# Performance work log

Hardware: AMD Instinct MI355X
Metric: run time of the kernel (lower is better)

The kernel has to match this reference:

```python
import jax, jax.numpy as jnp
import numpy as np

DIM = 256
HEADS = 8
HEAD_DIM = DIM // HEADS
EPS = 1e-5


def layer_norm(x, g, b):
    mu = jnp.mean(x, axis=-1, keepdims=True)
    var = jnp.mean(jnp.square(x - mu), axis=-1, keepdims=True)
    return (x - mu) * jax.lax.rsqrt(var + EPS) * g + b


def setup_inputs() -> dict:
    key = jax.random.key(0)
    ks = jax.random.split(key, 10)
    s = 0.02
    return {
        "x": jax.random.normal(ks[0], (4, DIM, 64, 64), dtype=jnp.float32),
        "g1": jnp.ones((DIM,), jnp.float32),
        "b1": jnp.zeros((DIM,), jnp.float32),
        "Wqkv": jax.random.normal(ks[1], (DIM, 3 * DIM), jnp.float32) * s,
        "Wp": jax.random.normal(ks[2], (DIM, DIM), jnp.float32) * s,
        "bp": jnp.zeros((DIM,), jnp.float32),
        "g2": jnp.ones((DIM,), jnp.float32),
        "b2": jnp.zeros((DIM,), jnp.float32),
        "W1": jax.random.normal(ks[3], (DIM, 2 * DIM), jnp.float32) * s,
        "bf1": jnp.zeros((2 * DIM,), jnp.float32),
        "W2": jax.random.normal(ks[4], (2 * DIM, DIM), jnp.float32) * s,
        "bf2": jnp.zeros((DIM,), jnp.float32),
    }


def reference(x, g1, b1, Wqkv, Wp, bp, g2, b2, W1, bf1, W2, bf2):
    B, C, H, W = x.shape
    N = H * W
    scale = HEAD_DIM ** -0.5
    tokens = x.reshape(B, C, N).transpose(0, 2, 1)  # [B,N,C]
    t = layer_norm(tokens, g1, b1)
    qkv = (t @ Wqkv).reshape(B, N, 3, HEADS, HEAD_DIM)
    q = qkv[:, :, 0].transpose(0, 2, 1, 3)  # [B,h,N,d]
    k = qkv[:, :, 1].transpose(0, 2, 1, 3)
    v = qkv[:, :, 2].transpose(0, 2, 1, 3)
    attn = jax.nn.softmax(jnp.einsum("bhnd,bhmd->bhnm", q, k) * scale, axis=-1)
    out = jnp.einsum("bhnm,bhmd->bhnd", attn, v)
    out = out.transpose(0, 2, 1, 3).reshape(B, N, C)
    tokens = tokens + out @ Wp + bp
    t2 = layer_norm(tokens, g2, b2)
    h = jax.nn.gelu(t2 @ W1 + bf1, approximate=False)
    tokens = tokens + h @ W2 + bf2
    return tokens.transpose(0, 2, 1).reshape(B, C, H, W)
```

## Files before the change

kernel.cpp:

```cpp
#include <hip/hip_runtime.h>

typedef unsigned short u16;
typedef unsigned int   u32;

using bf16x8 = __attribute__((ext_vector_type(8))) __bf16;
using f32x4  = __attribute__((ext_vector_type(4))) float;
using f32x16 = __attribute__((ext_vector_type(16))) float;

#define MFMA16(a, b, c) __builtin_amdgcn_mfma_f32_16x16x32_bf16((a), (b), (c), 0, 0, 0)
#define MFMA32(a, b, c) __builtin_amdgcn_mfma_f32_32x32x16_bf16((a), (b), (c), 0, 0, 0)

__device__ inline u16 f2bf(float f) {
  u32 x = __float_as_uint(f);
  return (u16)((x + 0x7FFFu + ((x >> 16) & 1u)) >> 16);
}

__device__ inline const bf16x8* bfp(const u16* p) {
  return reinterpret_cast<const bf16x8*>(p);
}

__global__ __launch_bounds__(256) void k_conv(
    const float* __restrict__ Wqkv, const float* __restrict__ Wp,
    const float* __restrict__ W1,   const float* __restrict__ W2,
    u16* __restrict__ wqkvT, u16* __restrict__ wpT,
    u16* __restrict__ w1T,   u16* __restrict__ w2T) {
  __shared__ float tile[32][33];
  int blk = blockIdx.x;
  const float* src; u16* dst; int R, C, t;
  if (blk < 192)      { src = Wqkv; dst = wqkvT; R = 256; C = 768; t = blk; }
  else if (blk < 256) { src = Wp;   dst = wpT;   R = 256; C = 256; t = blk - 192; }
  else if (blk < 384) { src = W1;   dst = w1T;   R = 256; C = 512; t = blk - 256; }
  else                { src = W2;   dst = w2T;   R = 512; C = 256; t = blk - 384; }
  int tpc = C >> 5;
  int tr = (t / tpc) << 5, tc = (t % tpc) << 5;
  int j = threadIdx.x & 31, iq = threadIdx.x >> 5;
  #pragma unroll
  for (int i = 0; i < 4; ++i)
    tile[iq + 8 * i][j] = src[(size_t)(tr + iq + 8 * i) * C + tc + j];
  __syncthreads();
  #pragma unroll
  for (int i = 0; i < 4; ++i)
    dst[(size_t)(tc + iq + 8 * i) * R + tr + j] = f2bf(tile[j][iq + 8 * i]);
}

__global__ __launch_bounds__(256) void k_ln1(
    const float* __restrict__ x, const float* __restrict__ g1,
    const float* __restrict__ b1, float* __restrict__ tokens,
    u16* __restrict__ ln) {
  __shared__ float tile[256][33];
  __shared__ float red[2][8][32];
  __shared__ float stat[2][32];
  int tid = threadIdx.x;
  int blk = blockIdx.x;
  int b = blk >> 7, n0 = (blk & 127) << 5;
  {
    int cq = tid >> 5, j = tid & 31;
    const float* xp = x + (((size_t)b * 256) << 12) + n0 + j;
    #pragma unroll 8
    for (int it = 0; it < 32; ++it) {
      int c = it * 8 + cq;
      tile[c][j] = xp[(size_t)c << 12];
    }
  }
  __syncthreads();
  {
    int tn = tid & 31, qq = tid >> 5;
    float s = 0.f, s2 = 0.f;
    #pragma unroll 8
    for (int i = 0; i < 32; ++i) {
      float v = tile[qq * 32 + i][tn];
      s += v; s2 += v * v;
    }
    red[0][qq][tn] = s; red[1][qq][tn] = s2;
  }
  __syncthreads();
  if (tid < 32) {
    float su = 0.f, sq = 0.f;
    #pragma unroll
    for (int qq = 0; qq < 8; ++qq) { su += red[0][qq][tid]; sq += red[1][qq][tid]; }
    float mu  = su * (1.f / 256.f);
    float var = sq * (1.f / 256.f) - mu * mu;
    stat[0][tid] = mu;
    stat[1][tid] = rsqrtf(var + 1e-5f);
  }
  __syncthreads();
  float g = g1[tid], bb = b1[tid];
  size_t base = ((size_t)(b * 4096 + n0)) * 256 + tid;
  for (int it = 0; it < 32; ++it) {
    float v = tile[tid][it];
    float y = (v - stat[0][it]) * stat[1][it] * g + bb;
    tokens[base + (size_t)it * 256] = v;
    ln[base + (size_t)it * 256] = f2bf(y);
  }
}

template <int K>
__device__ inline void mm16(const u16* __restrict__ A, const u16* __restrict__ BT,
                            int arow, int bcol, f32x4 acc[4]) {
  int lane = threadIdx.x & 63;
  int r = lane & 15, g = lane >> 4;
  const u16* ap  = A  + (size_t)(arow + r) * K + g * 8;
  const u16* bp0 = BT + (size_t)(bcol + r) * K + g * 8;
  #pragma unroll 4
  for (int k0 = 0; k0 < K; k0 += 32) {
    bf16x8 a = *bfp(ap + k0);
    #pragma unroll
    for (int nt = 0; nt < 4; ++nt) {
      bf16x8 b = *bfp(bp0 + nt * 16 * K + k0);
      acc[nt] = MFMA16(a, b, acc[nt]);
    }
  }
}

__global__ __launch_bounds__(256) void k_qkv(
    const u16* __restrict__ ln, const u16* __restrict__ wT,
    u16* __restrict__ q, u16* __restrict__ kf, u16* __restrict__ vf) {
  int w = threadIdx.x >> 6, lane = threadIdx.x & 63;
  int r16 = lane & 15, g4 = lane >> 4;
  int m0 = blockIdx.y * 64 + w * 16;
  int n0 = blockIdx.x * 64;
  f32x4 z = {0.f, 0.f, 0.f, 0.f};
  f32x4 acc[4] = {z, z, z, z};
  mm16<256>(ln, wT, m0, n0, acc);
  int b = m0 >> 12;
  int nbase = (m0 & 4095) + g4 * 4;
  const float qs = (float)(0.17677669529663687 * 1.4426950408889634);
  #pragma unroll
  for (int nt = 0; nt < 4; ++nt) {
    int col = n0 + nt * 16 + r16;
    int which = col >> 8, h = (col >> 5) & 7, d = col & 31;
    size_t bh_off = ((size_t)(b * 8 + h)) << 17;
    if (which == 0) {
      #pragma unroll
      for (int r = 0; r < 4; ++r)
        q[((size_t)(b * 8 + h) * 4096 + nbase + r) * 32 + d] = f2bf(acc[nt][r] * qs);
    } else if (which == 1) {
      int sel = d >> 4, lh = (d >> 3) & 1, jj = d & 7;
      #pragma unroll
      for (int r = 0; r < 4; ++r) {
        int key = nbase + r;
        kf[bh_off + (size_t)(key >> 5) * 1024 + sel * 512 +
           (((key & 31) | (lh << 5)) << 3) + jj] = f2bf(acc[nt][r]);
      }
    } else {
      int kk = nbase & 31;
      int sel = kk >> 4, lh = (kk >> 3) & 1, j0 = kk & 7;
      ushort4 o4;
      o4.x = f2bf(acc[nt][0]); o4.y = f2bf(acc[nt][1]);
      o4.z = f2bf(acc[nt][2]); o4.w = f2bf(acc[nt][3]);
      *(ushort4*)(vf + bh_off + (size_t)(nbase >> 5) * 1024 + sel * 512 +
                  ((d | (lh << 5)) << 3) + j0) = o4;
    }
  }
}

__global__ __launch_bounds__(512) void k_attn(
    const u16* __restrict__ q, const u16* __restrict__ kf,
    const u16* __restrict__ vf, u16* __restrict__ attnout) {
  __shared__ float obuf[4][64][17];
  __shared__ float lsbuf[4][64];
  int lane = threadIdx.x & 63;
  int w = threadIdx.x >> 6;
  int qi = w >> 1, kj = w & 1;
  int r32 = lane & 31, hi = lane >> 5;
  int bh = blockIdx.x >> 5;
  int qt = blockIdx.x & 31;
  int q0 = qt * 128 + qi * 32;
  const u16* qh = q + ((size_t)bh << 17);
  bf16x8 qf0 = *bfp(qh + (size_t)(q0 + r32) * 32 + hi * 8);
  bf16x8 qf1 = *bfp(qh + (size_t)(q0 + r32) * 32 + 16 + hi * 8);

  const u16* kp = kf + ((size_t)bh << 17) + (size_t)kj * 65536 + lane * 8;
  const u16* vp = vf + ((size_t)bh << 17) + (size_t)kj * 65536 + lane * 8;

  union { u32 u[4]; bf16x8 v; } ones;
  #pragma unroll
  for (int i = 0; i < 4; ++i) ones.u[i] = 0x3F803F80u;

  f32x16 o, ls, zz;
  #pragma unroll
  for (int r = 0; r < 16; ++r) { o[r] = 0.f; ls[r] = 0.f; zz[r] = 0.f; }

  #pragma unroll 2
  for (int c = 0; c < 64; ++c) {
    bf16x8 ka0 = *bfp(kp);
    bf16x8 ka1 = *bfp(kp + 512);
    bf16x8 va0 = *bfp(vp);
    bf16x8 va1 = *bfp(vp + 512);
    kp += 1024; vp += 1024;

    f32x16 s = MFMA32(ka0, qf0, zz);
    s = MFMA32(ka1, qf1, s);
    #pragma unroll
    for (int r = 0; r < 16; ++r) s[r] = __builtin_amdgcn_exp2f(s[r]);
    u32 c8[8];
    #pragma unroll
    for (int i = 0; i < 8; ++i)
      asm("v_cvt_pk_bf16_f32 %0, %1, %2" : "=v"(c8[i]) : "v"(s[2 * i]), "v"(s[2 * i + 1]));
    asm("v_permlane32_swap_b32 %0, %1" : "+v"(c8[0]), "+v"(c8[2]));
    asm("v_permlane32_swap_b32 %0, %1" : "+v"(c8[1]), "+v"(c8[3]));
    asm("v_permlane32_swap_b32 %0, %1" : "+v"(c8[4]), "+v"(c8[6]));
    asm("v_permlane32_swap_b32 %0, %1" : "+v"(c8[5]), "+v"(c8[7]));
    union { u32 u[4]; bf16x8 v; } pf0, pf1;
    pf0.u[0] = c8[0]; pf0.u[1] = c8[1]; pf0.u[2] = c8[2]; pf0.u[3] = c8[3];
    pf1.u[0] = c8[4]; pf1.u[1] = c8[5]; pf1.u[2] = c8[6]; pf1.u[3] = c8[7];
    ls = MFMA32(ones.v, pf0.v, ls);
    ls = MFMA32(ones.v, pf1.v, ls);
    o = MFMA32(va0, pf0.v, o);
    o = MFMA32(va1, pf1.v, o);
  }

  if (kj == 1) {
    #pragma unroll
    for (int g = 0; g < 16; ++g) obuf[qi][lane][g] = o[g];
    lsbuf[qi][lane] = ls[0];
  }
  __syncthreads();
  if (kj == 0) {
    float inv = __builtin_amdgcn_rcpf(ls[0] + lsbuf[qi][lane]);
    int b = bh >> 3, h = bh & 7;
    size_t nrow = ((size_t)(b * 4096 + q0 + r32)) * 256 + h * 32;
    #pragma unroll
    for (int g = 0; g < 4; ++g) {
      ushort4 ov;
      ov.x = f2bf((o[g * 4 + 0] + obuf[qi][lane][g * 4 + 0]) * inv);
      ov.y = f2bf((o[g * 4 + 1] + obuf[qi][lane][g * 4 + 1]) * inv);
      ov.z = f2bf((o[g * 4 + 2] + obuf[qi][lane][g * 4 + 2]) * inv);
      ov.w = f2bf((o[g * 4 + 3] + obuf[qi][lane][g * 4 + 3]) * inv);
      *(ushort4*)(attnout + nrow + g * 8 + hi * 4) = ov;
    }
  }
}

__global__ __launch_bounds__(256) void k_projln(
    const u16* __restrict__ ao, const u16* __restrict__ wT,
    const float* __restrict__ bp, const float* __restrict__ g2,
    const float* __restrict__ b2, float* __restrict__ tokens,
    u16* __restrict__ ln) {
  __shared__ float red[2][4][16];
  int w = threadIdx.x >> 6, lane = threadIdx.x & 63;
  int r16 = lane & 15, g4 = lane >> 4;
  int m0 = blockIdx.x * 16;
  int n0 = w * 64;
  f32x4 z = {0.f, 0.f, 0.f, 0.f};
  f32x4 acc[4] = {z, z, z, z};
  mm16<256>(ao, wT, m0, n0, acc);
  float sum[4] = {0.f, 0.f, 0.f, 0.f}, sq[4] = {0.f, 0.f, 0.f, 0.f};
  #pragma unroll
  for (int nt = 0; nt < 4; ++nt) {
    int col = n0 + nt * 16 + r16;
    float bias = bp[col];
    #pragma unroll
    for (int r = 0; r < 4; ++r) {
      float v = tokens[(size_t)(m0 + g4 * 4 + r) * 256 + col] + acc[nt][r] + bias;
      acc[nt][r] = v;
      sum[r] += v; sq[r] += v * v;
    }
  }
  #pragma unroll
  for (int mask = 1; mask < 16; mask <<= 1) {
    #pragma unroll
    for (int r = 0; r < 4; ++r) {
      sum[r] += __shfl_xor(sum[r], mask);
      sq[r]  += __shfl_xor(sq[r], mask);
    }
  }
  if (r16 == 0) {
    #pragma unroll
    for (int r = 0; r < 4; ++r) {
      red[0][w][g4 * 4 + r] = sum[r];
      red[1][w][g4 * 4 + r] = sq[r];
    }
  }
  __syncthreads();
  float mu[4], rs[4];
  #pragma unroll
  for (int r = 0; r < 4; ++r) {
    int ri = g4 * 4 + r;
    float S  = red[0][0][ri] + red[0][1][ri] + red[0][2][ri] + red[0][3][ri];
    float SQ = red[1][0][ri] + red[1][1][ri] + red[1][2][ri] + red[1][3][ri];
    mu[r] = S * (1.f / 256.f);
    rs[r] = rsqrtf(SQ * (1.f / 256.f) - mu[r] * mu[r] + 1e-5f);
  }
  #pragma unroll
  for (int nt = 0; nt < 4; ++nt) {
    int col = n0 + nt * 16 + r16;
    float gg = g2[col], bb = b2[col];
    #pragma unroll
    for (int r = 0; r < 4; ++r) {
      size_t idx = (size_t)(m0 + g4 * 4 + r) * 256 + col;
      float v = acc[nt][r];
      tokens[idx] = v;
      ln[idx] = f2bf((v - mu[r]) * rs[r] * gg + bb);
    }
  }
}

__global__ __launch_bounds__(512) void k_mlp(
    const u16* __restrict__ ln, const u16* __restrict__ w1T,
    const float* __restrict__ bf1, const u16* __restrict__ w2T,
    const float* __restrict__ bf2, const float* __restrict__ tokens,
    float* __restrict__ out) {
  __shared__ u16 hh[32][520];
  int w = threadIdx.x >> 6, lane = threadIdx.x & 63;
  int r16 = lane & 15, g4 = lane >> 4;
  int rh = w & 1, cg = w >> 1;
  int m0 = blockIdx.x * 32 + rh * 16;
  {
    f32x4 z = {0.f, 0.f, 0.f, 0.f};
    f32x4 acc[8] = {z, z, z, z, z, z, z, z};
    const u16* ap  = ln  + (size_t)(m0 + r16) * 256 + g4 * 8;
    const u16* bp0 = w1T + (size_t)(cg * 128 + r16) * 256 + g4 * 8;
    #pragma unroll 2
    for (int k0 = 0; k0 < 256; k0 += 32) {
      bf16x8 a = *bfp(ap + k0);
      #pragma unroll
      for (int nt = 0; nt < 8; ++nt) {
        bf16x8 b = *bfp(bp0 + nt * 16 * 256 + k0);
        acc[nt] = MFMA16(a, b, acc[nt]);
      }
    }
    int rl = rh * 16 + g4 * 4;
    #pragma unroll
    for (int nt = 0; nt < 8; ++nt) {
      int col = cg * 128 + nt * 16 + r16;
      float bias = bf1[col];
      #pragma unroll
      for (int r = 0; r < 4; ++r) {
        float xx = acc[nt][r] + bias;
        float x2 = xx * xx;
        float zt = xx * (2.3021188f + 0.10293855f * x2);
        float e  = __builtin_amdgcn_exp2f(zt);
        float ge = xx * (1.f - __builtin_amdgcn_rcpf(1.f + e));
        hh[rl + r][col] = f2bf(ge);
      }
    }
  }
  __syncthreads();
  f32x4 z = {0.f, 0.f, 0.f, 0.f};
  f32x4 acc[4] = {z, z, z, z};
  const u16* hrow = &hh[rh * 16 + r16][g4 * 8];
  const u16* bp2  = w2T + (size_t)(cg * 64 + r16) * 512 + g4 * 8;
  #pragma unroll 4
  for (int k0 = 0; k0 < 512; k0 += 32) {
    bf16x8 a = *bfp(hrow + k0);
    #pragma unroll
    for (int nt = 0; nt < 4; ++nt) {
      bf16x8 b = *bfp(bp2 + nt * 16 * 512 + k0);
      acc[nt] = MFMA16(a, b, acc[nt]);
    }
  }
  int b = m0 >> 12;
  int nl = (m0 & 4095) + g4 * 4;
  #pragma unroll
  for (int nt = 0; nt < 4; ++nt) {
    int col = cg * 64 + nt * 16 + r16;
    float bias = bf2[col];
    float4 o;
    o.x = tokens[(size_t)(m0 + g4 * 4 + 0) * 256 + col] + acc[nt][0] + bias;
    o.y = tokens[(size_t)(m0 + g4 * 4 + 1) * 256 + col] + acc[nt][1] + bias;
    o.z = tokens[(size_t)(m0 + g4 * 4 + 2) * 256 + col] + acc[nt][2] + bias;
    o.w = tokens[(size_t)(m0 + g4 * 4 + 3) * 256 + col] + acc[nt][3] + bias;
    *(float4*)(out + (((size_t)(b * 256 + col)) << 12) + nl) = o;
  }
}

extern "C" void kernel_launch(void* const* d_in, const int* in_sizes, int n_in,
                              void* d_out, int out_size, void* d_ws, size_t ws_size,
                              hipStream_t stream) {
  (void)in_sizes; (void)n_in; (void)out_size; (void)ws_size;
  const float* x    = (const float*)d_in[0];
  const float* g1   = (const float*)d_in[1];
  const float* b1   = (const float*)d_in[2];
  const float* Wqkv = (const float*)d_in[3];
  const float* Wp   = (const float*)d_in[4];
  const float* bp   = (const float*)d_in[5];
  const float* g2   = (const float*)d_in[6];
  const float* b2   = (const float*)d_in[7];
  const float* W1   = (const float*)d_in[8];
  const float* bf1  = (const float*)d_in[9];
  const float* W2   = (const float*)d_in[10];
  const float* bf2  = (const float*)d_in[11];
  float* out = (float*)d_out;

  char* ws = (char*)d_ws;
  float* tokens = (float*)(ws);
  u16* lnb      = (u16*)(ws + 16777216);
  u16* qb       = (u16*)(ws + 25165824);
  u16* kfb      = (u16*)(ws + 33554432);
  u16* vfb      = (u16*)(ws + 41943040);
  u16* aob      = (u16*)(ws + 50331648);
  u16* wqkvT    = (u16*)(ws + 67108864);
  u16* wpT      = (u16*)(ws + 67502080);
  u16* w1T      = (u16*)(ws + 67633152);
  u16* w2T      = (u16*)(ws + 67895296);

  k_conv  <<<512, 256, 0, stream>>>(Wqkv, Wp, W1, W2, wqkvT, wpT, w1T, w2T);
  k_ln1   <<<512, 256, 0, stream>>>(x, g1, b1, tokens, lnb);
  k_qkv   <<<dim3(12, 256), 256, 0, stream>>>(lnb, wqkvT, qb, kfb, vfb);
  k_attn  <<<1024, 512, 0, stream>>>(qb, kfb, vfb, aob);
  k_projln<<<1024, 256, 0, stream>>>(aob, wpT, bp, g2, b2, tokens, lnb);
  k_mlp   <<<512, 512, 0, stream>>>(lnb, w1T, bf1, w2T, bf2, tokens, out);
}
```

Before: 264.6 us.

## Enlarge QKV tile, prefetch K/V in attention, sum softmax row with VALU

The QKV GEMM now gives each wave 32 rows instead of 16, so every B fragment load feeds two MFMAs and the grid is halved. In the attention kernel, K/V fragments for the next chunk are loaded one iteration ahead (software pipelining). The two ones-vector MFMAs that built the row sum are replaced by VALU adds plus a cross-half shuffle. This cuts MFMA work and hides load latency in the hot attention loop, at the cost of extra registers and summing in fp32 instead of from bf16-rounded P.

```diff
diff --git a/kernel.cpp b/kernel.cpp
--- a/kernel.cpp
+++ b/kernel.cpp
@@ -112,44 +112,68 @@
   }
 }
 
+template <int K>
+__device__ inline void mm32(const u16* __restrict__ A, const u16* __restrict__ BT,
+                            int arow, int bcol, f32x4 acc[2][4]) {
+  int lane = threadIdx.x & 63;
+  int r = lane & 15, g = lane >> 4;
+  const u16* ap0 = A  + (size_t)(arow + r) * K + g * 8;
+  const u16* bp0 = BT + (size_t)(bcol + r) * K + g * 8;
+  #pragma unroll 4
+  for (int k0 = 0; k0 < K; k0 += 32) {
+    bf16x8 a0 = *bfp(ap0 + k0);
+    bf16x8 a1 = *bfp(ap0 + 16 * K + k0);
+    #pragma unroll
+    for (int nt = 0; nt < 4; ++nt) {
+      bf16x8 b = *bfp(bp0 + nt * 16 * K + k0);
+      acc[0][nt] = MFMA16(a0, b, acc[0][nt]);
+      acc[1][nt] = MFMA16(a1, b, acc[1][nt]);
+    }
+  }
+}
+
 __global__ __launch_bounds__(256) void k_qkv(
     const u16* __restrict__ ln, const u16* __restrict__ wT,
     u16* __restrict__ q, u16* __restrict__ kf, u16* __restrict__ vf) {
   int w = threadIdx.x >> 6, lane = threadIdx.x & 63;
   int r16 = lane & 15, g4 = lane >> 4;
-  int m0 = blockIdx.y * 64 + w * 16;
+  int m0 = blockIdx.y * 128 + w * 32;
   int n0 = blockIdx.x * 64;
   f32x4 z = {0.f, 0.f, 0.f, 0.f};
-  f32x4 acc[4] = {z, z, z, z};
-  mm16<256>(ln, wT, m0, n0, acc);
+  f32x4 acc[2][4] = {{z, z, z, z}, {z, z, z, z}};
+  mm32<256>(ln, wT, m0, n0, acc);
   int b = m0 >> 12;
-  int nbase = (m0 & 4095) + g4 * 4;
   const float qs = (float)(0.17677669529663687 * 1.4426950408889634);
   #pragma unroll
-  for (int nt = 0; nt < 4; ++nt) {
-    int col = n0 + nt * 16 + r16;
-    int which = col >> 8, h = (col >> 5) & 7, d = col & 31;
-    size_t bh_off = ((size_t)(b * 8 + h)) << 17;
-    if (which == 0) {
-      #pragma unroll
-      for (int r = 0; r < 4; ++r)
-        q[((size_t)(b * 8 + h) * 4096 + nbase + r) * 32 + d] = f2bf(acc[nt][r] * qs);
-    } else if (which == 1) {
-      int sel = d >> 4, lh = (d >> 3) & 1, jj = d & 7;
-      #pragma unroll
-      for (int r = 0; r < 4; ++r) {
-        int key = nbase + r;
-        kf[bh_off + (size_t)(key >> 5) * 1024 + sel * 512 +
-           (((key & 31) | (lh << 5)) << 3) + jj] = f2bf(acc[nt][r]);
+  for (int rg = 0; rg < 2; ++rg) {
+    int nbase = (m0 & 4095) + rg * 16 + g4 * 4;
+    #pragma unroll
+    for (int nt = 0; nt < 4; ++nt) {
+      int col = n0 + nt * 16 + r16;
+      int which = col >> 8, h = (col >> 5) & 7, d = col & 31;
+      size_t bh_off = ((size_t)(b * 8 + h)) << 17;
+      if (which == 0) {
+        #pragma unroll
+        for (int r = 0; r < 4; ++r)
+          q[((size_t)(b * 8 + h) * 4096 + nbase + r) * 32 + d] =
+              f2bf(acc[rg][nt][r] * qs);
+      } else if (which == 1) {
+        int sel = d >> 4, lh = (d >> 3) & 1, jj = d & 7;
+        #pragma unroll
+        for (int r = 0; r < 4; ++r) {
+          int key = nbase + r;
+          kf[bh_off + (size_t)(key >> 5) * 1024 + sel * 512 +
+             (((key & 31) | (lh << 5)) << 3) + jj] = f2bf(acc[rg][nt][r]);
+        }
+      } else {
+        int kk = nbase & 31;
+        int sel = kk >> 4, lh = (kk >> 3) & 1, j0 = kk & 7;
+        ushort4 o4;
+        o4.x = f2bf(acc[rg][nt][0]); o4.y = f2bf(acc[rg][nt][1]);
+        o4.z = f2bf(acc[rg][nt][2]); o4.w = f2bf(acc[rg][nt][3]);
+        *(ushort4*)(vf + bh_off + (size_t)(nbase >> 5) * 1024 + sel * 512 +
+                    ((d | (lh << 5)) << 3) + j0) = o4;
       }
-    } else {
-      int kk = nbase & 31;
-      int sel = kk >> 4, lh = (kk >> 3) & 1, j0 = kk & 7;
-      ushort4 o4;
-      o4.x = f2bf(acc[nt][0]); o4.y = f2bf(acc[nt][1]);
-      o4.z = f2bf(acc[nt][2]); o4.w = f2bf(acc[nt][3]);
-      *(ushort4*)(vf + bh_off + (size_t)(nbase >> 5) * 1024 + sel * 512 +
-                  ((d | (lh << 5)) << 3) + j0) = o4;
     }
   }
 }
@@ -173,26 +197,32 @@
   const u16* kp = kf + ((size_t)bh << 17) + (size_t)kj * 65536 + lane * 8;
   const u16* vp = vf + ((size_t)bh << 17) + (size_t)kj * 65536 + lane * 8;
 
-  union { u32 u[4]; bf16x8 v; } ones;
-  #pragma unroll
-  for (int i = 0; i < 4; ++i) ones.u[i] = 0x3F803F80u;
-
-  f32x16 o, ls, zz;
-  #pragma unroll
-  for (int r = 0; r < 16; ++r) { o[r] = 0.f; ls[r] = 0.f; zz[r] = 0.f; }
+  f32x16 o, zz;
+  #pragma unroll
+  for (int r = 0; r < 16; ++r) { o[r] = 0.f; zz[r] = 0.f; }
+  float lsum = 0.f;
+
+  bf16x8 ka0 = *bfp(kp);
+  bf16x8 ka1 = *bfp(kp + 512);
+  bf16x8 va0 = *bfp(vp);
+  bf16x8 va1 = *bfp(vp + 512);
+  kp += 1024; vp += 1024;
 
   #pragma unroll 2
   for (int c = 0; c < 64; ++c) {
-    bf16x8 ka0 = *bfp(kp);
-    bf16x8 ka1 = *bfp(kp + 512);
-    bf16x8 va0 = *bfp(vp);
-    bf16x8 va1 = *bfp(vp + 512);
+    bf16x8 kb0 = *bfp(kp);
+    bf16x8 kb1 = *bfp(kp + 512);
+    bf16x8 vb0 = *bfp(vp);
+    bf16x8 vb1 = *bfp(vp + 512);
     kp += 1024; vp += 1024;
 
     f32x16 s = MFMA32(ka0, qf0, zz);
     s = MFMA32(ka1, qf1, s);
     #pragma unroll
     for (int r = 0; r < 16; ++r) s[r] = __builtin_amdgcn_exp2f(s[r]);
+    float t0 = ((s[0] + s[1]) + (s[2] + s[3])) + ((s[4] + s[5]) + (s[6] + s[7]));
+    float t1 = ((s[8] + s[9]) + (s[10] + s[11])) + ((s[12] + s[13]) + (s[14] + s[15]));
+    lsum += t0 + t1;
     u32 c8[8];
     #pragma unroll
     for (int i = 0; i < 8; ++i)
@@ -204,20 +234,22 @@
     union { u32 u[4]; bf16x8 v; } pf0, pf1;
     pf0.u[0] = c8[0]; pf0.u[1] = c8[1]; pf0.u[2] = c8[2]; pf0.u[3] = c8[3];
     pf1.u[0] = c8[4]; pf1.u[1] = c8[5]; pf1.u[2] = c8[6]; pf1.u[3] = c8[7];
-    ls = MFMA32(ones.v, pf0.v, ls);
-    ls = MFMA32(ones.v, pf1.v, ls);
     o = MFMA32(va0, pf0.v, o);
     o = MFMA32(va1, pf1.v, o);
-  }
+
+    ka0 = kb0; ka1 = kb1; va0 = vb0; va1 = vb1;
+  }
+
+  lsum += __shfl_xor(lsum, 32);
 
   if (kj == 1) {
     #pragma unroll
     for (int g = 0; g < 16; ++g) obuf[qi][lane][g] = o[g];
-    lsbuf[qi][lane] = ls[0];
+    lsbuf[qi][lane] = lsum;
   }
   __syncthreads();
   if (kj == 0) {
-    float inv = __builtin_amdgcn_rcpf(ls[0] + lsbuf[qi][lane]);
+    float inv = __builtin_amdgcn_rcpf(lsum + lsbuf[qi][lane]);
     int b = bh >> 3, h = bh & 7;
     size_t nrow = ((size_t)(b * 4096 + q0 + r32)) * 256 + h * 32;
     #pragma unroll
@@ -397,7 +429,7 @@
 
   k_conv  <<<512, 256, 0, stream>>>(Wqkv, Wp, W1, W2, wqkvT, wpT, w1T, w2T);
   k_ln1   <<<512, 256, 0, stream>>>(x, g1, b1, tokens, lnb);
-  k_qkv   <<<dim3(12, 256), 256, 0, stream>>>(lnb, wqkvT, qb, kfb, vfb);
+  k_qkv   <<<dim3(12, 128), 256, 0, stream>>>(lnb, wqkvT, qb, kfb, vfb);
   k_attn  <<<1024, 512, 0, stream>>>(qb, kfb, vfb, aob);
   k_projln<<<1024, 256, 0, stream>>>(aob, wpT, bp, g2, b2, tokens, lnb);
   k_mlp   <<<512, 512, 0, stream>>>(lnb, w1T, bf1, w2T, bf2, tokens, out);
```

New measurement: 239.6 us. -9.4%, faster.
